# Optimization experiments

Hardware: AMD Instinct MI355X
Metric: run time of the kernel (lower is better)

The kernel has to match this reference:

```python
import jax, jax.numpy as jnp
import numpy as np

N_NODES = 50000
N_EDGES = 400000
IN_CH = 165
HID = 64
HEADS = 8
EPS = 1e-5
NEG_SLOPE = 0.2


def _layer_norm(x, g, b):
    mu = jnp.mean(x, axis=-1, keepdims=True)
    var = jnp.mean(jnp.square(x - mu), axis=-1, keepdims=True)
    return (x - mu) * jax.lax.rsqrt(var + EPS) * g + b


def _gat_conv(x, src, dst, W, a_src, a_dst, bias, concat):
    # x: [N, F_in]; src/dst: [E] (self-loops already appended)
    N = x.shape[0]
    H, C = a_src.shape
    h = (x @ W).reshape(N, H, C)                       # [N, H, C]
    alpha_s = jnp.sum(h * a_src, axis=-1)              # [N, H]
    alpha_d = jnp.sum(h * a_dst, axis=-1)              # [N, H]
    e = jax.nn.leaky_relu(alpha_s[src] + alpha_d[dst], NEG_SLOPE)  # [E, H]
    # segment softmax over incoming edges of each dst node
    m = jax.ops.segment_max(e, dst, num_segments=N)    # [N, H]
    m = jnp.where(jnp.isfinite(m), m, 0.0)
    ex = jnp.exp(e - m[dst])                           # [E, H]
    denom = jax.ops.segment_sum(ex, dst, num_segments=N)  # [N, H]
    alpha = ex / denom[dst]                            # [E, H]
    out = jax.ops.segment_sum(alpha[:, :, None] * h[src], dst, num_segments=N)  # [N, H, C]
    if concat:
        out = out.reshape(N, H * C)
    else:
        out = out.mean(axis=1)
    return out + bias


def setup_inputs() -> dict:
    key = jax.random.key(0)
    ks = jax.random.split(key, 24)
    sc = 0.05
    d = {
        'x': jax.random.normal(ks[0], (N_NODES, IN_CH), dtype=jnp.float32),
        'edge_index': jax.random.randint(ks[1], (2, N_EDGES), 0, N_NODES, dtype=jnp.int64),
        # layer 0: in=165 -> heads*hid=512 (concat)
        'W0': jax.random.normal(ks[2], (IN_CH, HEADS * HID), jnp.float32) * sc,
        'as0': jax.random.normal(ks[3], (HEADS, HID), jnp.float32) * sc,
        'ad0': jax.random.normal(ks[4], (HEADS, HID), jnp.float32) * sc,
        'b0': jnp.zeros((HEADS * HID,), jnp.float32),
        'lng0': jnp.ones((HEADS * HID,), jnp.float32),
        'lnb0': jnp.zeros((HEADS * HID,), jnp.float32),
        # layer 1: 512 -> 512 (concat, residual applies)
        'W1': jax.random.normal(ks[5], (HEADS * HID, HEADS * HID), jnp.float32) * sc,
        'as1': jax.random.normal(ks[6], (HEADS, HID), jnp.float32) * sc,
        'ad1': jax.random.normal(ks[7], (HEADS, HID), jnp.float32) * sc,
        'b1': jnp.zeros((HEADS * HID,), jnp.float32),
        'lng1': jnp.ones((HEADS * HID,), jnp.float32),
        'lnb1': jnp.zeros((HEADS * HID,), jnp.float32),
        # layer 2: 512 -> 64 (mean over heads)
        'W2': jax.random.normal(ks[8], (HEADS * HID, HEADS * HID), jnp.float32) * sc,
        'as2': jax.random.normal(ks[9], (HEADS, HID), jnp.float32) * sc,
        'ad2': jax.random.normal(ks[10], (HEADS, HID), jnp.float32) * sc,
        'b2': jnp.zeros((HID,), jnp.float32),
        'lng2': jnp.ones((HID,), jnp.float32),
        'lnb2': jnp.zeros((HID,), jnp.float32),
        'lin_w': jax.random.normal(ks[11], (HID, 2), jnp.float32) * sc,
        'lin_b': jnp.zeros((2,), jnp.float32),
    }
    return d


def reference(x, edge_index, W0, as0, ad0, b0, lng0, lnb0,
              W1, as1, ad1, b1, lng1, lnb1,
              W2, as2, ad2, b2, lng2, lnb2, lin_w, lin_b):
    N = x.shape[0]
    loops = jnp.arange(N, dtype=edge_index.dtype)
    src = jnp.concatenate([edge_index[0], loops])
    dst = jnp.concatenate([edge_index[1], loops])

    layers = [
        (W0, as0, ad0, b0, lng0, lnb0, True),
        (W1, as1, ad1, b1, lng1, lnb1, True),
        (W2, as2, ad2, b2, lng2, lnb2, False),
    ]
    h = x
    for (W, a_s, a_d, b, g, bb, concat) in layers:
        residual = h
        h = _gat_conv(h, src, dst, W, a_s, a_d, b, concat)
        if h.shape == residual.shape:
            h = h + residual
        h = _layer_norm(h, g, bb)
        h = jax.nn.relu(h)
        # dropout is identity in eval mode
    return h @ lin_w + lin_b
```

## Files before the change

### kernel.cpp

```cpp
#include <hip/hip_runtime.h>
#include <hip/hip_bf16.h>
#include <cstdint>
#include <cstddef>

#define HEADS 8
#define HID 64
#define HF 512
#define NEG_SLOPE 0.2f
#define LN_EPS 1e-5f

typedef __hip_bfloat16 bf16;
typedef __attribute__((ext_vector_type(8))) __bf16 bf16v8;
typedef __attribute__((ext_vector_type(4))) float f32x4;

__device__ __forceinline__ float wsum64(float v) {
#pragma unroll
  for (int o = 32; o > 0; o >>= 1) v += __shfl_xor(v, o, 64);
  return v;
}
__device__ __forceinline__ int wsum64i(int v) {
#pragma unroll
  for (int o = 32; o > 0; o >>= 1) v += __shfl_xor(v, o, 64);
  return v;
}
__device__ __forceinline__ float leaky(float v) { return v >= 0.f ? v : NEG_SLOPE * v; }
__device__ __forceinline__ float bits2f(unsigned short u) {
  return __uint_as_float(((unsigned)u) << 16);
}
__device__ __forceinline__ unsigned short f2bits(float x) {
  union { bf16 h; unsigned short u; } bu;
  bu.h = __float2bfloat16(x);
  return bu.u;
}
__device__ __forceinline__ void gload_lds16(const bf16* src, short* lds_base) {
  __builtin_amdgcn_global_load_lds(
      (const __attribute__((address_space(1))) unsigned int*)src,
      (__attribute__((address_space(3))) unsigned int*)lds_base, 16, 0, 0);
}

__global__ __launch_bounds__(256)
void convert_count(const int* __restrict__ ei, int* __restrict__ esrc,
                   int* __restrict__ edst, int* __restrict__ counts, int E) {
  int e = blockIdx.x * 256 + threadIdx.x;
  if (e >= E) return;
  bool i64 = (ei[1] == 0) && (ei[3] == 0) && (ei[5] == 0) && (ei[7] == 0);
  int s, d;
  if (i64) { s = ei[2 * (size_t)e]; d = ei[2 * ((size_t)E + e)]; }
  else     { s = ei[e];             d = ei[E + e]; }
  esrc[e] = s; edst[e] = d;
  atomicAdd(&counts[d], 1);
}

#define SCAN_T 256
#define SCAN_EPT 4
#define SCAN_CHUNK (SCAN_T * SCAN_EPT)

__global__ __launch_bounds__(SCAN_T)
void scan_pass1(const int* __restrict__ counts, int* __restrict__ bsum, int N) {
  int b = blockIdx.x, t = threadIdx.x;
  int base = b * SCAN_CHUNK + t * SCAN_EPT;
  int s = 0;
#pragma unroll
  for (int i = 0; i < SCAN_EPT; ++i) {
    int idx = base + i;
    if (idx < N) s += counts[idx] + 1;
  }
  int lane = t & 63, w = t >> 6;
  int tot = wsum64i(s);
  __shared__ int ws[4];
  if (lane == 0) ws[w] = tot;
  __syncthreads();
  if (t == 0) bsum[b] = ws[0] + ws[1] + ws[2] + ws[3];
}

__global__ __launch_bounds__(64)
void scan_pass2(const int* __restrict__ bsum, int* __restrict__ boff, int NB) {
  int t = threadIdx.x;
  int own = t < NB ? bsum[t] : 0;
  int v = own;
#pragma unroll
  for (int o = 1; o < 64; o <<= 1) {
    int u = __shfl_up(v, o, 64);
    if (t >= o) v += u;
  }
  if (t < NB) boff[t] = v - own;
}

__global__ __launch_bounds__(SCAN_T)
void scan_pass3(const int* __restrict__ counts, const int* __restrict__ boff,
                int* __restrict__ row_ptr, int* __restrict__ cursor, int N, int Etot) {
  int b = blockIdx.x, t = threadIdx.x;
  int base = b * SCAN_CHUNK + t * SCAN_EPT;
  int c[SCAN_EPT];
  int s = 0;
#pragma unroll
  for (int i = 0; i < SCAN_EPT; ++i) {
    int idx = base + i;
    c[i] = idx < N ? counts[idx] + 1 : 0;
    s += c[i];
  }
  int lane = t & 63, w = t >> 6;
  int inc = s;
#pragma unroll
  for (int o = 1; o < 64; o <<= 1) {
    int u = __shfl_up(inc, o, 64);
    if (lane >= o) inc += u;
  }
  __shared__ int wsums[4];
  if (lane == 63) wsums[w] = inc;
  __syncthreads();
  int woff = 0;
  for (int i = 0; i < w; ++i) woff += wsums[i];
  int run = inc - s + woff + boff[b];
#pragma unroll
  for (int i = 0; i < SCAN_EPT; ++i) {
    int idx = base + i;
    if (idx < N) { row_ptr[idx] = run; cursor[idx] = run; run += c[i]; }
  }
  if (b == 0 && t == 0) row_ptr[N] = Etot;
}

__global__ __launch_bounds__(256)
void scatter_kernel(const int* __restrict__ esrc, const int* __restrict__ edst,
                    int* __restrict__ cursor, int* __restrict__ col, int N, int E) {
  int e = blockIdx.x * 256 + threadIdx.x;
  int Etot = E + N;
  if (e >= Etot) return;
  int s = e < E ? esrc[e] : e - E;
  int d = e < E ? edst[e] : e - E;
  int pos = atomicAdd(&cursor[d], 1);
  col[pos] = s;
}

__global__ __launch_bounds__(256)
void convert_pad_x(const float* __restrict__ x, bf16* __restrict__ xbf,
                   int M, int K, int Kp) {
  int idx = blockIdx.x * 256 + threadIdx.x;
  if (idx >= M * Kp) return;
  int row = idx / Kp, colk = idx - row * Kp;
  float v = colk < K ? x[(size_t)row * K + colk] : 0.f;
  xbf[idx] = __float2bfloat16(v);
}

__global__ __launch_bounds__(256)
void transpose_w(const float* __restrict__ W, bf16* __restrict__ Wt,
                 int K, int Ncols, int Kp) {
  int idx = blockIdx.x * 256 + threadIdx.x;
  if (idx >= Ncols * Kp) return;
  int n = idx / Kp, k = idx - n * Kp;
  float v = k < K ? W[(size_t)k * Ncols + n] : 0.f;
  Wt[idx] = __float2bfloat16(v);
}

__global__ __launch_bounds__(256)
void gemm_mfma(const bf16* __restrict__ A, const bf16* __restrict__ Bt,
               bf16* __restrict__ C,
               const float* __restrict__ as_g, const float* __restrict__ ad_g,
               float* __restrict__ alpha_s, float* __restrict__ alpha_d,
               int M, int Ncols, int K) {
  __shared__ short Alds[128 * 32];
  __shared__ short Blds[128 * 32];
  const int tid = threadIdx.x;
  const int wave = tid >> 6, lane = tid & 63;
  const int wr = wave >> 1, wc = wave & 1;
  const int row0 = blockIdx.x * 128, col0 = blockIdx.y * 128;
  const int lrow = lane & 15;
  const int kc = lane >> 4;
  const int sr = lane >> 2, sc4 = lane & 3;
  f32x4 acc[4][4] = {};

  for (int k0 = 0; k0 < K; k0 += 32) {
#pragma unroll
    for (int i = 0; i < 2; ++i) {
      int rbase = (wave + i * 4) * 16;
      int r = rbase + sr;
      int slot = sc4 ^ ((r >> 1) & 3);
      int gm = row0 + r; if (gm >= M) gm = M - 1;
      gload_lds16(A + (size_t)gm * K + k0 + slot * 8, &Alds[rbase * 32]);
      gload_lds16(Bt + (size_t)(col0 + r) * K + k0 + slot * 8, &Blds[rbase * 32]);
    }
    __syncthreads();
    bf16v8 af[4], bfr[4];
#pragma unroll
    for (int r = 0; r < 4; ++r) {
      int row = wr * 64 + r * 16 + lrow;
      af[r] = *reinterpret_cast<const bf16v8*>(
          &Alds[row * 32 + ((kc ^ ((row >> 1) & 3)) << 3)]);
    }
#pragma unroll
    for (int c = 0; c < 4; ++c) {
      int row = wc * 64 + c * 16 + lrow;
      bfr[c] = *reinterpret_cast<const bf16v8*>(
          &Blds[row * 32 + ((kc ^ ((row >> 1) & 3)) << 3)]);
    }
#pragma unroll
    for (int r = 0; r < 4; ++r)
#pragma unroll
      for (int c = 0; c < 4; ++c)
        acc[r][c] = __builtin_amdgcn_mfma_f32_16x16x32_bf16(af[r], bfr[c], acc[r][c], 0, 0, 0);
    __syncthreads();
  }

  const int crow = (lane >> 4) * 4;
  const int ccol = lane & 15;
#pragma unroll
  for (int r = 0; r < 4; ++r) {
#pragma unroll
    for (int c = 0; c < 4; ++c) {
      int gc = col0 + wc * 64 + c * 16 + ccol;
#pragma unroll
      for (int j = 0; j < 4; ++j) {
        int gr = row0 + wr * 64 + r * 16 + crow + j;
        if (gr < M) C[(size_t)gr * Ncols + gc] = __float2bfloat16(acc[r][c][j]);
      }
    }
  }

  const int head = (col0 + wc * 64) >> 6;
  float asf[4], adf[4];
#pragma unroll
  for (int c = 0; c < 4; ++c) {
    asf[c] = as_g[head * HID + c * 16 + ccol];
    adf[c] = ad_g[head * HID + c * 16 + ccol];
  }
#pragma unroll
  for (int r = 0; r < 4; ++r) {
#pragma unroll
    for (int j = 0; j < 4; ++j) {
      float ps = 0.f, pd = 0.f;
#pragma unroll
      for (int c = 0; c < 4; ++c) {
        ps = fmaf(acc[r][c][j], asf[c], ps);
        pd = fmaf(acc[r][c][j], adf[c], pd);
      }
#pragma unroll
      for (int o = 1; o < 16; o <<= 1) {
        ps += __shfl_xor(ps, o, 64);
        pd += __shfl_xor(pd, o, 64);
      }
      if (ccol == 0) {
        int gr = row0 + wr * 64 + r * 16 + crow + j;
        if (gr < M) {
          alpha_s[gr * HEADS + head] = ps;
          alpha_d[gr * HEADS + head] = pd;
        }
      }
    }
  }
}

template <int LAYER>
__global__ __launch_bounds__(256)
void aggregate_kernel(const int* __restrict__ row_ptr, const int* __restrict__ col,
                      const bf16* __restrict__ hbuf,
                      const float* __restrict__ alpha_s, const float* __restrict__ alpha_d,
                      const bf16* __restrict__ resid,
                      const float* __restrict__ bias, const float* __restrict__ g,
                      const float* __restrict__ b,
                      bf16* __restrict__ out_bf, int N) {
  int w = threadIdx.x >> 6;
  int lane = threadIdx.x & 63;
  int nn = blockIdx.x * 4 + w;
  bool valid = nn < N;
  int n = valid ? nn : 0;
  int h = lane >> 3;
  float adh = alpha_d[n * HEADS + h];
  float m = -1e30f, den = 0.f;
  float a[8] = {};
  int lo = row_ptr[n], hi = row_ptr[n + 1];

  for (int j = lo; j < hi; j += 4) {
    int nrem = hi - j;
    int s0 = col[j];
    int s1 = col[nrem > 1 ? j + 1 : lo];
    int s2 = col[nrem > 2 ? j + 2 : lo];
    int s3 = col[nrem > 3 ? j + 3 : lo];
    float as0 = alpha_s[s0 * HEADS + h];
    float as1 = alpha_s[s1 * HEADS + h];
    float as2 = alpha_s[s2 * HEADS + h];
    float as3 = alpha_s[s3 * HEADS + h];
    uint4 u0 = *reinterpret_cast<const uint4*>(hbuf + (size_t)s0 * HF + lane * 8);
    uint4 u1 = *reinterpret_cast<const uint4*>(hbuf + (size_t)s1 * HF + lane * 8);
    uint4 u2 = *reinterpret_cast<const uint4*>(hbuf + (size_t)s2 * HF + lane * 8);
    uint4 u3 = *reinterpret_cast<const uint4*>(hbuf + (size_t)s3 * HF + lane * 8);
    float e0 = leaky(as0 + adh);
    float e1 = nrem > 1 ? leaky(as1 + adh) : -1e30f;
    float e2 = nrem > 2 ? leaky(as2 + adh) : -1e30f;
    float e3 = nrem > 3 ? leaky(as3 + adh) : -1e30f;
    float gmx = fmaxf(fmaxf(e0, e1), fmaxf(e2, e3));
    if (gmx > m) {
      float sc = __expf(m - gmx);
      den *= sc;
#pragma unroll
      for (int i = 0; i < 8; ++i) a[i] *= sc;
      m = gmx;
    }
    float x0 = __expf(e0 - m);
    float x1 = nrem > 1 ? __expf(e1 - m) : 0.f;
    float x2 = nrem > 2 ? __expf(e2 - m) : 0.f;
    float x3 = nrem > 3 ? __expf(e3 - m) : 0.f;
    den += (x0 + x1) + (x2 + x3);
    const unsigned short* p0 = reinterpret_cast<const unsigned short*>(&u0);
    const unsigned short* p1 = reinterpret_cast<const unsigned short*>(&u1);
    const unsigned short* p2 = reinterpret_cast<const unsigned short*>(&u2);
    const unsigned short* p3 = reinterpret_cast<const unsigned short*>(&u3);
#pragma unroll
    for (int i = 0; i < 8; ++i) {
      float t = fmaf(x0, bits2f(p0[i]), fmaf(x1, bits2f(p1[i]),
                fmaf(x2, bits2f(p2[i]), x3 * bits2f(p3[i]))));
      a[i] += t;
    }
  }
  float inv = 1.f / den;
#pragma unroll
  for (int i = 0; i < 8; ++i) a[i] *= inv;

  if (LAYER < 2) {
    float4 b0 = ((const float4*)bias)[lane * 2];
    float4 b1 = ((const float4*)bias)[lane * 2 + 1];
    a[0] += b0.x; a[1] += b0.y; a[2] += b0.z; a[3] += b0.w;
    a[4] += b1.x; a[5] += b1.y; a[6] += b1.z; a[7] += b1.w;
    if (LAYER == 1) {
      uint4 rr = *reinterpret_cast<const uint4*>(resid + (size_t)n * HF + lane * 8);
      const unsigned short* rs = reinterpret_cast<const unsigned short*>(&rr);
#pragma unroll
      for (int i = 0; i < 8; ++i) a[i] += bits2f(rs[i]);
    }
    float s = 0.f, ss = 0.f;
#pragma unroll
    for (int i = 0; i < 8; ++i) { s += a[i]; ss += a[i] * a[i]; }
    s = wsum64(s); ss = wsum64(ss);
    float mu = s * (1.f / HF);
    float var = ss * (1.f / HF) - mu * mu;
    float rs = rsqrtf(var + LN_EPS);
    float4 g0 = ((const float4*)g)[lane * 2], g1 = ((const float4*)g)[lane * 2 + 1];
    float4 e0 = ((const float4*)b)[lane * 2], e1 = ((const float4*)b)[lane * 2 + 1];
    float gg[8] = {g0.x, g0.y, g0.z, g0.w, g1.x, g1.y, g1.z, g1.w};
    float be[8] = {e0.x, e0.y, e0.z, e0.w, e1.x, e1.y, e1.z, e1.w};
    unsigned short o[8];
#pragma unroll
    for (int i = 0; i < 8; ++i)
      o[i] = f2bits(fmaxf((a[i] - mu) * rs * gg[i] + be[i], 0.f));
    if (valid)
      *reinterpret_cast<uint4*>(out_bf + (size_t)n * HF + lane * 8) =
          *reinterpret_cast<const uint4*>(o);
  } else {
    __shared__ float lds[4][HF];
#pragma unroll
    for (int i = 0; i < 8; ++i) lds[w][lane * 8 + i] = a[i];
    float v = 0.f;
#pragma unroll
    for (int hh = 0; hh < HEADS; ++hh) v += lds[w][hh * HID + lane];
    v = v * (1.f / HEADS) + bias[lane];
    float s = wsum64(v);
    float ss = wsum64(v * v);
    float mu = s * (1.f / HID);
    float var = ss * (1.f / HID) - mu * mu;
    float rs = rsqrtf(var + LN_EPS);
    v = fmaxf((v - mu) * rs * g[lane] + b[lane], 0.f);
    if (valid) out_bf[(size_t)n * HID + lane] = __float2bfloat16(v);
  }
}

__global__ __launch_bounds__(256)
void final_linear_kernel(const bf16* __restrict__ D, const float* __restrict__ w,
                         const float* __restrict__ bb, float* __restrict__ out, int N) {
  int wid = (blockIdx.x * 256 + threadIdx.x) >> 6;
  int lane = threadIdx.x & 63;
  if (wid >= N) return;
  float v = __bfloat162float(D[(size_t)wid * HID + lane]);
  float s0 = wsum64(v * w[lane * 2 + 0]);
  float s1 = wsum64(v * w[lane * 2 + 1]);
  if (lane == 0) {
    out[(size_t)wid * 2 + 0] = s0 + bb[0];
    out[(size_t)wid * 2 + 1] = s1 + bb[1];
  }
}

extern "C" void kernel_launch(void* const* d_in, const int* in_sizes, int n_in,
                              void* d_out, int out_size, void* d_ws, size_t ws_size,
                              hipStream_t stream) {
  const float* x  = (const float*)d_in[0];
  const int*   ei = (const int*)d_in[1];
  const int N = in_sizes[0] / 165;
  const int E = in_sizes[1] / 2;
  const int Etot = E + N;
  const int K0P = 192;

  const float* W[3]  = {(const float*)d_in[2],  (const float*)d_in[8],  (const float*)d_in[14]};
  const float* As[3] = {(const float*)d_in[3],  (const float*)d_in[9],  (const float*)d_in[15]};
  const float* Ad[3] = {(const float*)d_in[4],  (const float*)d_in[10], (const float*)d_in[16]};
  const float* Bi[3] = {(const float*)d_in[5],  (const float*)d_in[11], (const float*)d_in[17]};
  const float* Lg[3] = {(const float*)d_in[6],  (const float*)d_in[12], (const float*)d_in[18]};
  const float* Lb[3] = {(const float*)d_in[7],  (const float*)d_in[13], (const float*)d_in[19]};
  const float* lin_w = (const float*)d_in[20];
  const float* lin_b = (const float*)d_in[21];

  char* p = (char*)d_ws;
  auto alloc = [&](size_t bytes) {
    char* r = p;
    p += (bytes + 255) & ~(size_t)255;
    return r;
  };
  bf16* feat0   = (bf16*)alloc((size_t)N * HF * 2);
  bf16* hbuf    = (bf16*)alloc((size_t)N * HF * 2);
  bf16* bufD    = (bf16*)alloc((size_t)N * HID * 2);
  float* alpha_s = (float*)alloc((size_t)N * HEADS * 4);
  float* alpha_d = (float*)alloc((size_t)N * HEADS * 4);
  bf16* W0t = (bf16*)alloc((size_t)HF * K0P * 2);
  bf16* W1t = (bf16*)alloc((size_t)HF * HF * 2);
  bf16* W2t = (bf16*)alloc((size_t)HF * HF * 2);
  int* esrc    = (int*)alloc((size_t)E * 4);
  int* edst    = (int*)alloc((size_t)E * 4);
  int* counts  = (int*)alloc((size_t)N * 4);
  int* row_ptr = (int*)alloc((size_t)(N + 1) * 4);
  int* cursor  = (int*)alloc((size_t)N * 4);
  int* col     = (int*)alloc((size_t)Etot * 4);
  int* bsum    = (int*)alloc((size_t)256 * 4);
  int* boff    = (int*)alloc((size_t)256 * 4);
  (void)ws_size;

  bf16* xbf = feat0;

  const int NB = (N + SCAN_CHUNK - 1) / SCAN_CHUNK;

  hipMemsetAsync(counts, 0, (size_t)N * 4, stream);
  convert_count<<<(E + 255) / 256, 256, 0, stream>>>(ei, esrc, edst, counts, E);
  scan_pass1<<<NB, SCAN_T, 0, stream>>>(counts, bsum, N);
  scan_pass2<<<1, 64, 0, stream>>>(bsum, boff, NB);
  scan_pass3<<<NB, SCAN_T, 0, stream>>>(counts, boff, row_ptr, cursor, N, Etot);
  scatter_kernel<<<(Etot + 255) / 256, 256, 0, stream>>>(esrc, edst, cursor, col, N, E);

  convert_pad_x<<<((N * K0P) + 255) / 256, 256, 0, stream>>>(x, xbf, N, 165, K0P);
  transpose_w<<<((HF * K0P) + 255) / 256, 256, 0, stream>>>(W[0], W0t, 165, HF, K0P);
  transpose_w<<<((HF * HF) + 255) / 256, 256, 0, stream>>>(W[1], W1t, HF, HF, HF);
  transpose_w<<<((HF * HF) + 255) / 256, 256, 0, stream>>>(W[2], W2t, HF, HF, HF);

  dim3 ggrid((N + 127) / 128, HF / 128);
  const int aggBlocks  = (N + 3) / 4;
  const int waveBlocks = (N + 3) / 4;

  gemm_mfma<<<ggrid, 256, 0, stream>>>(xbf, W0t, hbuf, As[0], Ad[0],
                                       alpha_s, alpha_d, N, HF, K0P);
  aggregate_kernel<0><<<aggBlocks, 256, 0, stream>>>(row_ptr, col, hbuf, alpha_s, alpha_d,
                                                     nullptr, Bi[0], Lg[0], Lb[0], feat0, N);

  gemm_mfma<<<ggrid, 256, 0, stream>>>(feat0, W1t, hbuf, As[1], Ad[1],
                                       alpha_s, alpha_d, N, HF, HF);
  aggregate_kernel<1><<<aggBlocks, 256, 0, stream>>>(row_ptr, col, hbuf, alpha_s, alpha_d,
                                                     feat0, Bi[1], Lg[1], Lb[1], feat0, N);

  gemm_mfma<<<ggrid, 256, 0, stream>>>(feat0, W2t, hbuf, As[2], Ad[2],
                                       alpha_s, alpha_d, N, HF, HF);
  aggregate_kernel<2><<<aggBlocks, 256, 0, stream>>>(row_ptr, col, hbuf, alpha_s, alpha_d,
                                                     nullptr, Bi[2], Lg[2], Lb[2], bufD, N);

  final_linear_kernel<<<waveBlocks, 256, 0, stream>>>(bufD, lin_w, lin_b, (float*)d_out, N);
}
```

Before: 477.0 us.

## Fuse prep kernels, remap GEMM blocks per XCD, unroll aggregation by 8, fuse final linear

```diff
diff --git a/kernel.cpp b/kernel.cpp
--- a/kernel.cpp
+++ b/kernel.cpp
@@ -133,23 +133,39 @@
 }
 
 __global__ __launch_bounds__(256)
-void convert_pad_x(const float* __restrict__ x, bf16* __restrict__ xbf,
-                   int M, int K, int Kp) {
+void prep_kernel(const float* __restrict__ x, bf16* __restrict__ xbf,
+                 const float* __restrict__ W0, bf16* __restrict__ W0t,
+                 const float* __restrict__ W1, bf16* __restrict__ W1t,
+                 const float* __restrict__ W2, bf16* __restrict__ W2t,
+                 int N, int K0P) {
+  const int S0 = N * K0P;
+  const int S1 = HF * K0P;
+  const int S2 = HF * HF;
   int idx = blockIdx.x * 256 + threadIdx.x;
-  if (idx >= M * Kp) return;
-  int row = idx / Kp, colk = idx - row * Kp;
-  float v = colk < K ? x[(size_t)row * K + colk] : 0.f;
-  xbf[idx] = __float2bfloat16(v);
-}
-
-__global__ __launch_bounds__(256)
-void transpose_w(const float* __restrict__ W, bf16* __restrict__ Wt,
-                 int K, int Ncols, int Kp) {
-  int idx = blockIdx.x * 256 + threadIdx.x;
-  if (idx >= Ncols * Kp) return;
-  int n = idx / Kp, k = idx - n * Kp;
-  float v = k < K ? W[(size_t)k * Ncols + n] : 0.f;
-  Wt[idx] = __float2bfloat16(v);
+  if (idx < S0) {
+    int row = idx / K0P, colk = idx - row * K0P;
+    float v = colk < 165 ? x[(size_t)row * 165 + colk] : 0.f;
+    xbf[idx] = __float2bfloat16(v);
+    return;
+  }
+  idx -= S0;
+  if (idx < S1) {
+    int n = idx / K0P, k = idx - n * K0P;
+    float v = k < 165 ? W0[(size_t)k * HF + n] : 0.f;
+    W0t[idx] = __float2bfloat16(v);
+    return;
+  }
+  idx -= S1;
+  if (idx < S2) {
+    int n = idx >> 9, k = idx & 511;
+    W1t[idx] = __float2bfloat16(W1[(size_t)k * HF + n]);
+    return;
+  }
+  idx -= S2;
+  if (idx < S2) {
+    int n = idx >> 9, k = idx & 511;
+    W2t[idx] = __float2bfloat16(W2[(size_t)k * HF + n]);
+  }
 }
 
 __global__ __launch_bounds__(256)
@@ -157,13 +173,20 @@
                bf16* __restrict__ C,
                const float* __restrict__ as_g, const float* __restrict__ ad_g,
                float* __restrict__ alpha_s, float* __restrict__ alpha_d,
-               int M, int Ncols, int K) {
+               int M, int Ncols, int K, int RT) {
+  const int id = blockIdx.x;
+  const int xcd = id & 7;
+  const int q = id >> 3;
+  const int cco = q & 3;
+  const int rt = (q >> 2) * 8 + xcd;
+  if (rt >= RT) return;
+  const int row0 = rt * 128, col0 = cco * 128;
+
   __shared__ short Alds[128 * 32];
   __shared__ short Blds[128 * 32];
   const int tid = threadIdx.x;
   const int wave = tid >> 6, lane = tid & 63;
   const int wr = wave >> 1, wc = wave & 1;
-  const int row0 = blockIdx.x * 128, col0 = blockIdx.y * 128;
   const int lrow = lane & 15;
   const int kc = lane >> 4;
   const int sr = lane >> 2, sc4 = lane & 3;
@@ -257,7 +280,8 @@
                       const bf16* __restrict__ resid,
                       const float* __restrict__ bias, const float* __restrict__ g,
                       const float* __restrict__ b,
-                      bf16* __restrict__ out_bf, int N) {
+                      const float* __restrict__ lw, const float* __restrict__ lb,
+                      bf16* __restrict__ out_bf, float* __restrict__ out_f, int N) {
   int w = threadIdx.x >> 6;
   int lane = threadIdx.x & 63;
   int nn = blockIdx.x * 4 + w;
@@ -269,25 +293,21 @@
   float a[8] = {};
   int lo = row_ptr[n], hi = row_ptr[n + 1];
 
-  for (int j = lo; j < hi; j += 4) {
-    int nrem = hi - j;
-    int s0 = col[j];
-    int s1 = col[nrem > 1 ? j + 1 : lo];
-    int s2 = col[nrem > 2 ? j + 2 : lo];
-    int s3 = col[nrem > 3 ? j + 3 : lo];
-    float as0 = alpha_s[s0 * HEADS + h];
-    float as1 = alpha_s[s1 * HEADS + h];
-    float as2 = alpha_s[s2 * HEADS + h];
-    float as3 = alpha_s[s3 * HEADS + h];
-    uint4 u0 = *reinterpret_cast<const uint4*>(hbuf + (size_t)s0 * HF + lane * 8);
-    uint4 u1 = *reinterpret_cast<const uint4*>(hbuf + (size_t)s1 * HF + lane * 8);
-    uint4 u2 = *reinterpret_cast<const uint4*>(hbuf + (size_t)s2 * HF + lane * 8);
-    uint4 u3 = *reinterpret_cast<const uint4*>(hbuf + (size_t)s3 * HF + lane * 8);
-    float e0 = leaky(as0 + adh);
-    float e1 = nrem > 1 ? leaky(as1 + adh) : -1e30f;
-    float e2 = nrem > 2 ? leaky(as2 + adh) : -1e30f;
-    float e3 = nrem > 3 ? leaky(as3 + adh) : -1e30f;
-    float gmx = fmaxf(fmaxf(e0, e1), fmaxf(e2, e3));
+  for (int j = lo; j < hi; j += 8) {
+    int idx[8]; float as[8]; uint4 u[8]; float e[8];
+#pragma unroll
+    for (int k = 0; k < 8; ++k) idx[k] = col[(j + k < hi) ? j + k : lo];
+#pragma unroll
+    for (int k = 0; k < 8; ++k) as[k] = alpha_s[idx[k] * HEADS + h];
+#pragma unroll
+    for (int k = 0; k < 8; ++k)
+      u[k] = *reinterpret_cast<const uint4*>(hbuf + (size_t)idx[k] * HF + lane * 8);
+#pragma unroll
+    for (int k = 0; k < 8; ++k)
+      e[k] = (j + k < hi) ? leaky(as[k] + adh) : -1e30f;
+    float m01 = fmaxf(e[0], e[1]), m23 = fmaxf(e[2], e[3]);
+    float m45 = fmaxf(e[4], e[5]), m67 = fmaxf(e[6], e[7]);
+    float gmx = fmaxf(fmaxf(m01, m23), fmaxf(m45, m67));
     if (gmx > m) {
       float sc = __expf(m - gmx);
       den *= sc;
@@ -295,20 +315,16 @@
       for (int i = 0; i < 8; ++i) a[i] *= sc;
       m = gmx;
     }
-    float x0 = __expf(e0 - m);
-    float x1 = nrem > 1 ? __expf(e1 - m) : 0.f;
-    float x2 = nrem > 2 ? __expf(e2 - m) : 0.f;
-    float x3 = nrem > 3 ? __expf(e3 - m) : 0.f;
-    den += (x0 + x1) + (x2 + x3);
-    const unsigned short* p0 = reinterpret_cast<const unsigned short*>(&u0);
-    const unsigned short* p1 = reinterpret_cast<const unsigned short*>(&u1);
-    const unsigned short* p2 = reinterpret_cast<const unsigned short*>(&u2);
-    const unsigned short* p3 = reinterpret_cast<const unsigned short*>(&u3);
-#pragma unroll
-    for (int i = 0; i < 8; ++i) {
-      float t = fmaf(x0, bits2f(p0[i]), fmaf(x1, bits2f(p1[i]),
-                fmaf(x2, bits2f(p2[i]), x3 * bits2f(p3[i]))));
-      a[i] += t;
+    float xk[8];
+#pragma unroll
+    for (int k = 0; k < 8; ++k) xk[k] = __expf(e[k] - m);
+#pragma unroll
+    for (int k = 0; k < 8; ++k) den += xk[k];
+#pragma unroll
+    for (int k = 0; k < 8; ++k) {
+      const unsigned short* pk = reinterpret_cast<const unsigned short*>(&u[k]);
+#pragma unroll
+      for (int i = 0; i < 8; ++i) a[i] = fmaf(xk[k], bits2f(pk[i]), a[i]);
     }
   }
   float inv = 1.f / den;
@@ -358,22 +374,12 @@
     float var = ss * (1.f / HID) - mu * mu;
     float rs = rsqrtf(var + LN_EPS);
     v = fmaxf((v - mu) * rs * g[lane] + b[lane], 0.f);
-    if (valid) out_bf[(size_t)n * HID + lane] = __float2bfloat16(v);
-  }
-}
-
-__global__ __launch_bounds__(256)
-void final_linear_kernel(const bf16* __restrict__ D, const float* __restrict__ w,
-                         const float* __restrict__ bb, float* __restrict__ out, int N) {
-  int wid = (blockIdx.x * 256 + threadIdx.x) >> 6;
-  int lane = threadIdx.x & 63;
-  if (wid >= N) return;
-  float v = __bfloat162float(D[(size_t)wid * HID + lane]);
-  float s0 = wsum64(v * w[lane * 2 + 0]);
-  float s1 = wsum64(v * w[lane * 2 + 1]);
-  if (lane == 0) {
-    out[(size_t)wid * 2 + 0] = s0 + bb[0];
-    out[(size_t)wid * 2 + 1] = s1 + bb[1];
+    float s0 = wsum64(v * lw[lane * 2 + 0]);
+    float s1 = wsum64(v * lw[lane * 2 + 1]);
+    if (valid && lane == 0) {
+      out_f[(size_t)n * 2 + 0] = s0 + lb[0];
+      out_f[(size_t)n * 2 + 1] = s1 + lb[1];
+    }
   }
 }
 
@@ -404,7 +410,6 @@
   };
   bf16* feat0   = (bf16*)alloc((size_t)N * HF * 2);
   bf16* hbuf    = (bf16*)alloc((size_t)N * HF * 2);
-  bf16* bufD    = (bf16*)alloc((size_t)N * HID * 2);
   float* alpha_s = (float*)alloc((size_t)N * HEADS * 4);
   float* alpha_d = (float*)alloc((size_t)N * HEADS * 4);
   bf16* W0t = (bf16*)alloc((size_t)HF * K0P * 2);
@@ -431,29 +436,32 @@
   scan_pass3<<<NB, SCAN_T, 0, stream>>>(counts, boff, row_ptr, cursor, N, Etot);
   scatter_kernel<<<(Etot + 255) / 256, 256, 0, stream>>>(esrc, edst, cursor, col, N, E);
 
-  convert_pad_x<<<((N * K0P) + 255) / 256, 256, 0, stream>>>(x, xbf, N, 165, K0P);
-  transpose_w<<<((HF * K0P) + 255) / 256, 256, 0, stream>>>(W[0], W0t, 165, HF, K0P);
-  transpose_w<<<((HF * HF) + 255) / 256, 256, 0, stream>>>(W[1], W1t, HF, HF, HF);
-  transpose_w<<<((HF * HF) + 255) / 256, 256, 0, stream>>>(W[2], W2t, HF, HF, HF);
-
-  dim3 ggrid((N + 127) / 128, HF / 128);
+  {
+    int total = N * K0P + HF * K0P + 2 * HF * HF;
+    prep_kernel<<<(total + 255) / 256, 256, 0, stream>>>(
+        x, xbf, W[0], W0t, W[1], W1t, W[2], W2t, N, K0P);
+  }
+
+  const int RT  = (N + 127) / 128;
+  const int RTp = ((RT + 7) / 8) * 8;
+  const int gemmBlocks = RTp * 4;
   const int aggBlocks  = (N + 3) / 4;
-  const int waveBlocks = (N + 3) / 4;
-
-  gemm_mfma<<<ggrid, 256, 0, stream>>>(xbf, W0t, hbuf, As[0], Ad[0],
-                                       alpha_s, alpha_d, N, HF, K0P);
+
+  gemm_mfma<<<gemmBlocks, 256, 0, stream>>>(xbf, W0t, hbuf, As[0], Ad[0],
+                                            alpha_s, alpha_d, N, HF, K0P, RT);
   aggregate_kernel<0><<<aggBlocks, 256, 0, stream>>>(row_ptr, col, hbuf, alpha_s, alpha_d,
-                                                     nullptr, Bi[0], Lg[0], Lb[0], feat0, N);
-
-  gemm_mfma<<<ggrid, 256, 0, stream>>>(feat0, W1t, hbuf, As[1], Ad[1],
-                                       alpha_s, alpha_d, N, HF, HF);
+                                                     nullptr, Bi[0], Lg[0], Lb[0],
+                                                     nullptr, nullptr, feat0, nullptr, N);
+
+  gemm_mfma<<<gemmBlocks, 256, 0, stream>>>(feat0, W1t, hbuf, As[1], Ad[1],
+                                            alpha_s, alpha_d, N, HF, HF, RT);
   aggregate_kernel<1><<<aggBlocks, 256, 0, stream>>>(row_ptr, col, hbuf, alpha_s, alpha_d,
-                                                     feat0, Bi[1], Lg[1], Lb[1], feat0, N);
-
-  gemm_mfma<<<ggrid, 256, 0, stream>>>(feat0, W2t, hbuf, As[2], Ad[2],
-                                       alpha_s, alpha_d, N, HF, HF);
+                                                     feat0, Bi[1], Lg[1], Lb[1],
+                                                     nullptr, nullptr, feat0, nullptr, N);
+
+  gemm_mfma<<<gemmBlocks, 256, 0, stream>>>(feat0, W2t, hbuf, As[2], Ad[2],
+                                            alpha_s, alpha_d, N, HF, HF, RT);
   aggregate_kernel<2><<<aggBlocks, 256, 0, stream>>>(row_ptr, col, hbuf, alpha_s, alpha_d,
-                                                     nullptr, Bi[2], Lg[2], Lb[2], bufD, N);
-
-  final_linear_kernel<<<waveBlocks, 256, 0, stream>>>(bufD, lin_w, lin_b, (float*)d_out, N);
-}
+                                                     nullptr, Bi[2], Lg[2], Lb[2],
+                                                     lin_w, lin_b, nullptr, (float*)d_out, N);
+}
```

Measured after the change: 439.5 us. -7.9%, faster.
